# Kernel tuning notes

Hardware: AMD Instinct MI355X
Metric: run time of the kernel (lower is better)

## Reference

```python
import jax, jax.numpy as jnp
import numpy as np

B, S, NX, H = 8, 1024, 1024, 16
HD = NX // H  # head dim = 64
MASKED_BIAS = -10000.0


def setup_inputs() -> dict:
    key = jax.random.key(0)
    ks = jax.random.split(key, 6)
    return {
        "x": jax.random.normal(ks[0], (B, S, NX), dtype=jnp.float32),
        "query": jax.random.normal(ks[1], (B, S, NX), dtype=jnp.float32),
        "c_attn_w": jax.random.normal(ks[2], (NX, 3 * NX), dtype=jnp.float32) * 0.02,
        "c_attn_b": jnp.zeros((3 * NX,), dtype=jnp.float32),
        "c_proj_w": jax.random.normal(ks[3], (NX, NX), dtype=jnp.float32) * 0.02,
        "c_proj_b": jnp.zeros((NX,), dtype=jnp.float32),
    }


def _split_heads(t):
    # [B, S, NX] -> [B, H, S, HD]
    b, s, _ = t.shape
    return t.reshape(b, s, H, HD).transpose(0, 2, 1, 3)


def reference(x, query, c_attn_w, c_attn_b, c_proj_w, c_proj_b):
    # Conv1D: y = x @ W + b
    kv = x @ c_attn_w + c_attn_b          # [B,S,3NX]; use key/value slices
    qy = query @ c_attn_w + c_attn_b      # [B,S,3NX]; use query slice
    q = _split_heads(qy[..., :NX])                     # [B,H,S,HD]
    k = _split_heads(kv[..., NX:2 * NX])               # [B,H,S,HD]
    v = _split_heads(kv[..., 2 * NX:])                 # [B,H,S,HD]

    w = jnp.einsum("bhqd,bhkd->bhqk", q, k) / jnp.sqrt(jnp.float32(HD))
    causal = jnp.tril(jnp.ones((S, S), dtype=bool))[None, None]
    w = jnp.where(causal, w, jnp.float32(MASKED_BIAS))
    w = jax.nn.softmax(w, axis=-1)
    a = jnp.einsum("bhqk,bhkd->bhqd", w, v)            # [B,H,S,HD]
    a = a.transpose(0, 2, 1, 3).reshape(B, S, NX)      # merge heads
    return a @ c_proj_w + c_proj_b
```

## Files before the change

### kernel.cpp

```cpp
#include <hip/hip_runtime.h>
#include <cstdint>
#include <cstddef>

#define Bb   8
#define Ss   1024
#define NXx  1024
#define Hh   16
#define HDd  64
#define Mm   (Bb*Ss)

typedef __bf16 bf16x8 __attribute__((ext_vector_type(8)));
typedef float  f32x4  __attribute__((ext_vector_type(4)));

__device__ __forceinline__ unsigned short f2bf(float f) {
    union { float f; unsigned int u; } v; v.f = f;
    return (unsigned short)((v.u + 0x8000u) >> 16);
}

__device__ __forceinline__ unsigned cvt_pk_bf16(float lo, float hi) {
    unsigned r;
    asm("v_cvt_pk_bf16_f32 %0, %1, %2" : "=v"(r) : "v"(lo), "v"(hi));
    return r;
}

__device__ __forceinline__ void load_lds16(const unsigned short* g, unsigned short* lds_base) {
    __builtin_amdgcn_global_load_lds(
        (const __attribute__((address_space(1))) void*)g,
        (__attribute__((address_space(3))) void*)lds_base, 16, 0, 0);
}

__global__ __launch_bounds__(256) void prep(
    const float* __restrict__ x, const float* __restrict__ query,
    const float* __restrict__ caw, const float* __restrict__ cpw,
    unsigned short* __restrict__ xb, unsigned short* __restrict__ qb,
    unsigned short* __restrict__ Wt, unsigned short* __restrict__ Pt)
{
    __shared__ float tile[32][33];
    const int bid = blockIdx.x;
    const int tid = threadIdx.x;

    if (bid < 16384) {
        const float* in = (bid < 8192) ? x : query;
        unsigned short* out = (bid < 8192) ? xb : qb;
        const int i = ((bid & 8191) * 256 + tid) * 4;
        const float4 v = *(const float4*)(in + i);
        unsigned long long p = (unsigned long long)f2bf(v.x)
            | ((unsigned long long)f2bf(v.y) << 16)
            | ((unsigned long long)f2bf(v.z) << 32)
            | ((unsigned long long)f2bf(v.w) << 48);
        *(unsigned long long*)(out + i) = p;
        return;
    }

    const float* in;
    unsigned short* out;
    int C, t;
    if (bid < 16384 + 3072) { in = caw; out = Wt; C = 3072; t = bid - 16384; }
    else                    { in = cpw; out = Pt; C = 1024; t = bid - 19456; }
    const int ntx = C >> 5;
    const int c0 = (t % ntx) * 32, r0 = (t / ntx) * 32;
    const int tx = tid & 31, ty = tid >> 5;
    for (int i = ty; i < 32; i += 8)
        tile[i][tx] = in[(size_t)(r0 + i) * C + c0 + tx];
    __syncthreads();
    for (int i = ty; i < 32; i += 8)
        out[(size_t)(c0 + i) * 1024 + r0 + tx] = f2bf(tile[tx][i]);
}

__global__ __launch_bounds__(512, 4) void gemm256(
    const unsigned short* __restrict__ Ax,
    const unsigned short* __restrict__ Aq,
    const unsigned short* __restrict__ Bt,
    const float* __restrict__ bias,
    unsigned short* __restrict__ out_q,
    unsigned short* __restrict__ out_k,
    unsigned short* __restrict__ out_v)
{
    __shared__ unsigned short lds[36864];

    const int tid  = threadIdx.x;
    const int w    = tid >> 6;
    const int lane = tid & 63;
    const int wm   = (w >> 1) * 64;
    const int wn   = (w & 1) * 64;
    const int lrow = lane & 15;
    const int quad = lane >> 4;
    const int ph   = (quad ^ (lrow & 3) ^ (lrow >> 2)) & 3;

    const int n    = blockIdx.x;
    const int xcd  = n & 7;
    const int sg   = n >> 3;
    const int mi   = (xcd >> 1) * 8 + sg / 12;
    const int ni   = (xcd & 1) * 12 + sg % 12;
    const int m0   = mi << 8;
    const int n0   = ni << 7;
    const int region = n0 >> 10;
    const unsigned short* A = (region == 0) ? Aq : Ax;

    const int srow = lane >> 2;
    const int scol = (((lane & 3) ^ (srow & 3) ^ ((srow >> 2) & 3)) << 3);
    const unsigned short* pA0 = A  + (size_t)(m0 + w * 32 + srow) * 1024 + scol;
    const unsigned short* pA1 = A  + (size_t)(m0 + w * 32 + 16 + srow) * 1024 + scol;
    const unsigned short* pB0 = Bt + (size_t)(n0 + w * 16 + srow) * 1024 + scol;

    f32x4 acc[4][4] = {};

#pragma unroll
    for (int p = 0; p < 2; ++p) {
        const int bb = p * 12288;
        load_lds16(pA0, lds + bb + w * 1024);
        load_lds16(pA1, lds + bb + w * 1024 + 512);
        load_lds16(pB0, lds + bb + 8192 + w * 512);
        pA0 += 32; pA1 += 32; pB0 += 32;
    }
    asm volatile("s_waitcnt vmcnt(3)" ::: "memory");

    int cbuf = 0;
    int sbuf = 2;
#pragma unroll 1
    for (int t = 0; t < 32; ++t) {
        __builtin_amdgcn_s_barrier();
        asm volatile("" ::: "memory");
        if (t <= 29) {
            const int bb = sbuf * 12288;
            load_lds16(pA0, lds + bb + w * 1024);
            load_lds16(pA1, lds + bb + w * 1024 + 512);
            load_lds16(pB0, lds + bb + 8192 + w * 512);
            pA0 += 32; pA1 += 32; pB0 += 32;
        }

        const int rA = cbuf * 12288 + (wm + lrow) * 32 + ph * 8;
        const int rB = cbuf * 12288 + 8192 + (wn + lrow) * 32 + ph * 8;
        bf16x8 af[4], bq[4];
#pragma unroll
        for (int i = 0; i < 4; ++i) af[i] = *(const bf16x8*)&lds[rA + i * 512];
#pragma unroll
        for (int j = 0; j < 4; ++j) bq[j] = *(const bf16x8*)&lds[rB + j * 512];
        __builtin_amdgcn_s_setprio(1);
#pragma unroll
        for (int i = 0; i < 4; ++i)
#pragma unroll
            for (int j = 0; j < 4; ++j)
                acc[i][j] = __builtin_amdgcn_mfma_f32_16x16x32_bf16(af[i], bq[j], acc[i][j], 0, 0, 0);
        __builtin_amdgcn_s_setprio(0);

        if (t <= 29)      asm volatile("s_waitcnt vmcnt(3)" ::: "memory");
        else if (t == 30) asm volatile("s_waitcnt vmcnt(0)" ::: "memory");

        cbuf = (cbuf == 2) ? 0 : cbuf + 1;
        sbuf = (sbuf == 2) ? 0 : sbuf + 1;
    }

    __syncthreads();

    unsigned short* ep = lds + w * 2048;

    if (region != 2) {
        unsigned short* outp = (region == 0) ? out_q : out_k;
        const float sc = (region == 0) ? 0.125f : 1.0f;
#pragma unroll
        for (int j = 0; j < 4; ++j) {
            const float bv = bias[n0 + wn + j * 16 + lrow];
#pragma unroll
            for (int i = 0; i < 4; ++i)
#pragma unroll
                for (int r = 0; r < 4; ++r)
                    ep[(i * 16 + quad * 4 + r) * 24 + lrow] = f2bf((acc[i][j][r] + bv) * sc);
#pragma unroll
            for (int tt = 0; tt < 2; ++tt) {
                const int c    = tt * 64 + lane;
                const int row  = c >> 1, ch = (c & 1) * 8;
                const int mrow = m0 + wm + row;
                const int cc   = (n0 + wn + j * 16 + ch) & (NXx - 1);
                const int hh   = cc >> 6, dd = cc & 63;
                const int bh   = (mrow >> 10) * Hh + hh;
                const int ss   = mrow & (Ss - 1);
                *(uint4*)&outp[((size_t)bh * Ss + ss) * HDd + dd] =
                    *(const uint4*)&ep[row * 24 + ch];
            }
        }
    } else {
#pragma unroll
        for (int j = 0; j < 4; ++j) {
            const float bv = bias[n0 + wn + j * 16 + lrow];
#pragma unroll
            for (int i = 0; i < 4; ++i)
#pragma unroll
                for (int r = 0; r < 4; ++r)
                    ep[lrow * 72 + i * 16 + quad * 4 + r] = f2bf(acc[i][j][r] + bv);
#pragma unroll
            for (int tt = 0; tt < 2; ++tt) {
                const int c    = tt * 64 + lane;
                const int col  = c >> 3, rc = (c & 7) * 8;
                const int cc   = (n0 + wn + j * 16 + col) & (NXx - 1);
                const int hh   = cc >> 6, dd = cc & 63;
                const int mrow = m0 + wm + rc;
                const int bh   = (mrow >> 10) * Hh + hh;
                const int ss   = mrow & (Ss - 1);
                *(uint4*)&out_v[((size_t)bh * HDd + dd) * Ss + ss] =
                    *(const uint4*)&ep[col * 72 + rc];
            }
        }
    }
}

__global__ __launch_bounds__(512, 4) void gemmp(
    const unsigned short* __restrict__ A,
    const unsigned short* __restrict__ Bt,
    const float* __restrict__ bias,
    float* __restrict__ out_f)
{
    __shared__ unsigned short lds[24576];

    const int tid  = threadIdx.x;
    const int w    = tid >> 6;
    const int lane = tid & 63;
    const int wm   = (w >> 1) * 32;
    const int wn   = (w & 1) * 64;
    const int lrow = lane & 15;
    const int quad = lane >> 4;
    const int ph   = (quad ^ (lrow & 3) ^ (lrow >> 2)) & 3;

    const int n    = blockIdx.x;
    const int xcd  = n & 7;
    const int sg   = n >> 3;
    const int mi   = (xcd >> 1) * 16 + sg / 4;
    const int ni   = (xcd & 1) * 4 + (sg & 3);
    const int m0   = mi << 7;
    const int n0   = ni << 7;

    const int srow = lane >> 2;
    const int scol = (((lane & 3) ^ (srow & 3) ^ ((srow >> 2) & 3)) << 3);
    const unsigned short* pA0 = A  + (size_t)(m0 + w * 16 + srow) * 1024 + scol;
    const unsigned short* pB0 = Bt + (size_t)(n0 + w * 16 + srow) * 1024 + scol;

    f32x4 acc[2][4] = {};

#pragma unroll
    for (int p = 0; p < 2; ++p) {
        const int bb = p * 8192;
        load_lds16(pA0, lds + bb + w * 512);
        load_lds16(pB0, lds + bb + 4096 + w * 512);
        pA0 += 32; pB0 += 32;
    }
    asm volatile("s_waitcnt vmcnt(2)" ::: "memory");

    int cbuf = 0, sbuf = 2;
#pragma unroll 1
    for (int t = 0; t < 32; ++t) {
        __builtin_amdgcn_s_barrier();
        asm volatile("" ::: "memory");
        if (t <= 29) {
            const int bb = sbuf * 8192;
            load_lds16(pA0, lds + bb + w * 512);
            load_lds16(pB0, lds + bb + 4096 + w * 512);
            pA0 += 32; pB0 += 32;
        }

        const int rA = cbuf * 8192 + (wm + lrow) * 32 + ph * 8;
        const int rB = cbuf * 8192 + 4096 + (wn + lrow) * 32 + ph * 8;
        bf16x8 af[2], bq[4];
#pragma unroll
        for (int i = 0; i < 2; ++i) af[i] = *(const bf16x8*)&lds[rA + i * 512];
#pragma unroll
        for (int j = 0; j < 4; ++j) bq[j] = *(const bf16x8*)&lds[rB + j * 512];
        __builtin_amdgcn_s_setprio(1);
#pragma unroll
        for (int i = 0; i < 2; ++i)
#pragma unroll
            for (int j = 0; j < 4; ++j)
                acc[i][j] = __builtin_amdgcn_mfma_f32_16x16x32_bf16(af[i], bq[j], acc[i][j], 0, 0, 0);
        __builtin_amdgcn_s_setprio(0);

        if (t <= 29)      asm volatile("s_waitcnt vmcnt(2)" ::: "memory");
        else if (t == 30) asm volatile("s_waitcnt vmcnt(0)" ::: "memory");

        cbuf = (cbuf == 2) ? 0 : cbuf + 1;
        sbuf = (sbuf == 2) ? 0 : sbuf + 1;
    }

#pragma unroll
    for (int i = 0; i < 2; ++i)
#pragma unroll
        for (int j = 0; j < 4; ++j) {
            const int ncol = n0 + wn + j * 16 + lrow;
            const float bv = bias[ncol];
#pragma unroll
            for (int r = 0; r < 4; ++r) {
                const int mrow = m0 + wm + i * 16 + quad * 4 + r;
                out_f[(size_t)mrow * NXx + ncol] = acc[i][j][r] + bv;
            }
        }
}

__global__ __launch_bounds__(512) void flash_attn(
    const unsigned short* __restrict__ Qh,
    const unsigned short* __restrict__ Kh,
    const unsigned short* __restrict__ Vt,
    unsigned short* __restrict__ about)
{
    __shared__ unsigned short Ks[3][64][64];
    __shared__ unsigned short Vs[3][64][64];
    __shared__ unsigned short Pl[8][32][72];

    const int tid  = threadIdx.x;
    const int w    = tid >> 6;
    const int lane = tid & 63;
    const int bh   = blockIdx.x & 127;
    const int prg  = blockIdx.x >> 7;
    const int b    = bh >> 4, h = bh & 15;
    const int lrow = lane & 15;
    const int quad = lane >> 4;

    const unsigned short* Qb = Qh + (size_t)bh * Ss * HDd;
    const unsigned short* Kb = Kh + (size_t)bh * Ss * HDd;
    const unsigned short* Vb = Vt + (size_t)bh * HDd * Ss;

    const int sr = lane >> 3;
    const int lc = (((lane & 7) ^ sr) << 3);

    const int swz = lrow & 7;
    const int ca = ((quad ^ swz) << 3);
    const int cb = (((4 + quad) ^ swz) << 3);

    const int nkt0 = 4 * prg + 4;
    int qw = prg * 256 + w * 32;

    bf16x8 aq[2][2];
#pragma unroll
    for (int g = 0; g < 2; ++g)
#pragma unroll
        for (int c = 0; c < 2; ++c)
            aq[g][c] = *(const bf16x8*)(Qb + (size_t)(qw + g * 16 + lrow) * HDd + c * 32 + quad * 8);

    f32x4 O[2][4] = {};
    float lsum[2] = { 0.f, 0.f };

#pragma unroll
    for (int p = 0; p < 2; ++p) {
        load_lds16(Kb + (size_t)(p * 64 + w * 8 + sr) * HDd + lc, &Ks[p][w * 8][0]);
        load_lds16(Vb + (size_t)(w * 8 + sr) * Ss + p * 64 + lc,  &Vs[p][w * 8][0]);
    }
    asm volatile("s_waitcnt vmcnt(2)" ::: "memory");

    int cbuf = 0, sbuf = 2;
#pragma unroll 1
    for (int it = 0; it < 20; ++it) {
        __builtin_amdgcn_s_barrier();
        asm volatile("" ::: "memory");
        if (it <= 17) {
            const int itn = it + 2;
            const int k0n = (itn >= nkt0 ? itn - nkt0 : itn) * 64;
            load_lds16(Kb + (size_t)(k0n + w * 8 + sr) * HDd + lc, &Ks[sbuf][w * 8][0]);
            load_lds16(Vb + (size_t)(w * 8 + sr) * Ss + k0n + lc,  &Vs[sbuf][w * 8][0]);
        }

        if (it == nkt0) {
#pragma unroll
            for (int g = 0; g < 2; ++g) {
                float l = lsum[g];
                l += __shfl_xor(l, 16);
                l += __shfl_xor(l, 32);
                const float inv = 1.0f / l;
#pragma unroll
                for (int r = 0; r < 4; ++r) {
                    const float invr = __shfl(inv, quad * 4 + r);
                    const int q = qw + g * 16 + quad * 4 + r;
                    const size_t base = ((size_t)b * Ss + q) * NXx + h * HDd;
#pragma unroll
                    for (int f = 0; f < 4; ++f)
                        about[base + f * 16 + lrow] = f2bf(O[g][f][r] * invr);
                }
            }
            qw = (3 - prg) * 256 + w * 32;
#pragma unroll
            for (int g = 0; g < 2; ++g)
#pragma unroll
                for (int c = 0; c < 2; ++c)
                    aq[g][c] = *(const bf16x8*)(Qb + (size_t)(qw + g * 16 + lrow) * HDd + c * 32 + quad * 8);
#pragma unroll
            for (int g = 0; g < 2; ++g) {
                lsum[g] = 0.f;
#pragma unroll
                for (int f = 0; f < 4; ++f) O[g][f] = (f32x4){0.f, 0.f, 0.f, 0.f};
            }
        }

        const int k0 = (it >= nkt0 ? it - nkt0 : it) * 64;
        if (k0 <= qw + 31) {
            f32x4 st[2][4] = {};
#pragma unroll
            for (int j = 0; j < 4; ++j) {
                const bf16x8 kf0 = *(const bf16x8*)&Ks[cbuf][j * 16 + lrow][ca];
                const bf16x8 kf1 = *(const bf16x8*)&Ks[cbuf][j * 16 + lrow][cb];
                st[0][j] = __builtin_amdgcn_mfma_f32_16x16x32_bf16(kf0, aq[0][0], st[0][j], 0, 0, 0);
                st[0][j] = __builtin_amdgcn_mfma_f32_16x16x32_bf16(kf1, aq[0][1], st[0][j], 0, 0, 0);
                st[1][j] = __builtin_amdgcn_mfma_f32_16x16x32_bf16(kf0, aq[1][0], st[1][j], 0, 0, 0);
                st[1][j] = __builtin_amdgcn_mfma_f32_16x16x32_bf16(kf1, aq[1][1], st[1][j], 0, 0, 0);
            }

            const bool needMask = (k0 + 63 > qw);
#pragma unroll
            for (int g = 0; g < 2; ++g) {
                const int qg = qw + g * 16 + lrow;
#pragma unroll
                for (int j = 0; j < 4; ++j) {
                    const int kbase = k0 + j * 16 + quad * 4;
                    float e0 = __expf(st[g][j][0]);
                    float e1 = __expf(st[g][j][1]);
                    float e2 = __expf(st[g][j][2]);
                    float e3 = __expf(st[g][j][3]);
                    if (needMask) {
                        if (kbase     > qg) e0 = 0.f;
                        if (kbase + 1 > qg) e1 = 0.f;
                        if (kbase + 2 > qg) e2 = 0.f;
                        if (kbase + 3 > qg) e3 = 0.f;
                    }
                    lsum[g] += (e0 + e1) + (e2 + e3);
                    uint2 pk;
                    pk.x = cvt_pk_bf16(e0, e1);
                    pk.y = cvt_pk_bf16(e2, e3);
                    *(uint2*)&Pl[w][g * 16 + lrow][j * 16 + quad * 4] = pk;
                }
            }

            bf16x8 ap[2][2];
#pragma unroll
            for (int g = 0; g < 2; ++g)
#pragma unroll
                for (int c = 0; c < 2; ++c)
                    ap[g][c] = *(const bf16x8*)&Pl[w][g * 16 + lrow][c * 32 + quad * 8];
#pragma unroll
            for (int f = 0; f < 4; ++f) {
                const bf16x8 vf0 = *(const bf16x8*)&Vs[cbuf][f * 16 + lrow][ca];
                const bf16x8 vf1 = *(const bf16x8*)&Vs[cbuf][f * 16 + lrow][cb];
                O[0][f] = __builtin_amdgcn_mfma_f32_16x16x32_bf16(ap[0][0], vf0, O[0][f], 0, 0, 0);
                O[0][f] = __builtin_amdgcn_mfma_f32_16x16x32_bf16(ap[0][1], vf1, O[0][f], 0, 0, 0);
                O[1][f] = __builtin_amdgcn_mfma_f32_16x16x32_bf16(ap[1][0], vf0, O[1][f], 0, 0, 0);
                O[1][f] = __builtin_amdgcn_mfma_f32_16x16x32_bf16(ap[1][1], vf1, O[1][f], 0, 0, 0);
            }
        }

        if (it <= 17)      asm volatile("s_waitcnt vmcnt(2)" ::: "memory");
        else if (it == 18) asm volatile("s_waitcnt vmcnt(0)" ::: "memory");

        cbuf = (cbuf == 2) ? 0 : cbuf + 1;
        sbuf = (sbuf == 2) ? 0 : sbuf + 1;
    }

#pragma unroll
    for (int g = 0; g < 2; ++g) {
        float l = lsum[g];
        l += __shfl_xor(l, 16);
        l += __shfl_xor(l, 32);
        const float inv = 1.0f / l;
#pragma unroll
        for (int r = 0; r < 4; ++r) {
            const float invr = __shfl(inv, quad * 4 + r);
            const int q = qw + g * 16 + quad * 4 + r;
            const size_t base = ((size_t)b * Ss + q) * NXx + h * HDd;
#pragma unroll
            for (int f = 0; f < 4; ++f)
                about[base + f * 16 + lrow] = f2bf(O[g][f][r] * invr);
        }
    }
}

extern "C" void kernel_launch(void* const* d_in, const int* in_sizes, int n_in,
                              void* d_out, int out_size, void* d_ws, size_t ws_size,
                              hipStream_t stream) {
    const float* x        = (const float*)d_in[0];
    const float* query    = (const float*)d_in[1];
    const float* c_attn_w = (const float*)d_in[2];
    const float* c_attn_b = (const float*)d_in[3];
    const float* c_proj_w = (const float*)d_in[4];
    const float* c_proj_b = (const float*)d_in[5];
    float* out = (float*)d_out;

    const size_t nTok = (size_t)Mm * NXx;
    char* ws = (char*)d_ws;
    unsigned short* xb    = (unsigned short*)ws;                 ws += nTok * 2;
    unsigned short* qb    = (unsigned short*)ws;                 ws += nTok * 2;
    unsigned short* Wt    = (unsigned short*)ws;                 ws += (size_t)3 * NXx * NXx * 2;
    unsigned short* Pt    = (unsigned short*)ws;                 ws += (size_t)NXx * NXx * 2;
    unsigned short* Qh    = (unsigned short*)ws;                 ws += nTok * 2;
    unsigned short* Kh    = (unsigned short*)ws;                 ws += nTok * 2;
    unsigned short* Vt    = (unsigned short*)ws;                 ws += nTok * 2;
    unsigned short* about = (unsigned short*)ws;                 ws += nTok * 2;
    if ((size_t)(ws - (char*)d_ws) > ws_size) return;

    prep<<<20480, 256, 0, stream>>>(x, query, c_attn_w, c_proj_w, xb, qb, Wt, Pt);

    gemm256<<<768, 512, 0, stream>>>(xb, qb, Wt, c_attn_b, Qh, Kh, Vt);

    flash_attn<<<256, 512, 0, stream>>>(Qh, Kh, Vt, about);

    gemmp<<<512, 512, 0, stream>>>(about, Pt, c_proj_b, out);
}
```

Before: 262.2 us.

## Replace projection GEMM with 256-thread single-buffered kernel; move flash-attn waits before barrier

The output projection GEMM moves from a 512-thread, triple-buffered, 32-wide-K pipeline to a 256-thread kernel. Each wave now computes a 64x64 tile over K=64 steps, loading into a single XOR-swizzled LDS buffer between two __syncthreads. This gives more MFMA work per LDS load and fewer waves, but removes the overlap of global loads with compute. In flash attention, the vmcnt waits move before a second barrier placed after the prefetch issue, so the current tile is confirmed resident before compute. This adds a barrier per iteration.

```diff
diff --git a/kernel.cpp b/kernel.cpp
--- a/kernel.cpp
+++ b/kernel.cpp
@@ -204,83 +204,69 @@
     }
 }
 
-__global__ __launch_bounds__(512, 4) void gemmp(
+__global__ __launch_bounds__(256) void gemm128p(
     const unsigned short* __restrict__ A,
     const unsigned short* __restrict__ Bt,
     const float* __restrict__ bias,
     float* __restrict__ out_f)
 {
-    __shared__ unsigned short lds[24576];
+    __shared__ unsigned short smem[16384];
+    unsigned short (*As)[64] = (unsigned short (*)[64])(smem);
+    unsigned short (*Bs)[64] = (unsigned short (*)[64])(smem + 8192);
 
     const int tid  = threadIdx.x;
     const int w    = tid >> 6;
     const int lane = tid & 63;
-    const int wm   = (w >> 1) * 32;
+
+    const int n    = blockIdx.x;
+    const int xcd  = n & 7;
+    const int sgrp = n >> 3;
+    const int m0   = ((xcd >> 1) * 16 + sgrp / 4) * 128;
+    const int n0   = ((xcd & 1) * 4 + sgrp % 4) * 128;
+
+    const int wm   = (w >> 1) * 64;
     const int wn   = (w & 1) * 64;
     const int lrow = lane & 15;
     const int quad = lane >> 4;
-    const int ph   = (quad ^ (lrow & 3) ^ (lrow >> 2)) & 3;
-
-    const int n    = blockIdx.x;
-    const int xcd  = n & 7;
-    const int sg   = n >> 3;
-    const int mi   = (xcd >> 1) * 16 + sg / 4;
-    const int ni   = (xcd & 1) * 4 + (sg & 3);
-    const int m0   = mi << 7;
-    const int n0   = ni << 7;
-
-    const int srow = lane >> 2;
-    const int scol = (((lane & 3) ^ (srow & 3) ^ ((srow >> 2) & 3)) << 3);
-    const unsigned short* pA0 = A  + (size_t)(m0 + w * 16 + srow) * 1024 + scol;
-    const unsigned short* pB0 = Bt + (size_t)(n0 + w * 16 + srow) * 1024 + scol;
-
-    f32x4 acc[2][4] = {};
-
-#pragma unroll
-    for (int p = 0; p < 2; ++p) {
-        const int bb = p * 8192;
-        load_lds16(pA0, lds + bb + w * 512);
-        load_lds16(pB0, lds + bb + 4096 + w * 512);
-        pA0 += 32; pB0 += 32;
-    }
-    asm volatile("s_waitcnt vmcnt(2)" ::: "memory");
-
-    int cbuf = 0, sbuf = 2;
-#pragma unroll 1
-    for (int t = 0; t < 32; ++t) {
-        __builtin_amdgcn_s_barrier();
-        asm volatile("" ::: "memory");
-        if (t <= 29) {
-            const int bb = sbuf * 8192;
-            load_lds16(pA0, lds + bb + w * 512);
-            load_lds16(pB0, lds + bb + 4096 + w * 512);
-            pA0 += 32; pB0 += 32;
-        }
-
-        const int rA = cbuf * 8192 + (wm + lrow) * 32 + ph * 8;
-        const int rB = cbuf * 8192 + 4096 + (wn + lrow) * 32 + ph * 8;
-        bf16x8 af[2], bq[4];
-#pragma unroll
-        for (int i = 0; i < 2; ++i) af[i] = *(const bf16x8*)&lds[rA + i * 512];
-#pragma unroll
-        for (int j = 0; j < 4; ++j) bq[j] = *(const bf16x8*)&lds[rB + j * 512];
-        __builtin_amdgcn_s_setprio(1);
-#pragma unroll
-        for (int i = 0; i < 2; ++i)
-#pragma unroll
-            for (int j = 0; j < 4; ++j)
-                acc[i][j] = __builtin_amdgcn_mfma_f32_16x16x32_bf16(af[i], bq[j], acc[i][j], 0, 0, 0);
-        __builtin_amdgcn_s_setprio(0);
-
-        if (t <= 29)      asm volatile("s_waitcnt vmcnt(2)" ::: "memory");
-        else if (t == 30) asm volatile("s_waitcnt vmcnt(0)" ::: "memory");
-
-        cbuf = (cbuf == 2) ? 0 : cbuf + 1;
-        sbuf = (sbuf == 2) ? 0 : sbuf + 1;
-    }
-
-#pragma unroll
-    for (int i = 0; i < 2; ++i)
+
+    f32x4 acc[4][4] = {};
+
+    const int rr   = lane >> 3;
+    const int scol = (((lane & 7) ^ (lane >> 3)) << 3);
+    const unsigned short* Ag = A  + (size_t)(m0 + w * 32 + rr) * 1024 + scol;
+    const unsigned short* Bg = Bt + (size_t)(n0 + w * 32 + rr) * 1024 + scol;
+    unsigned short* ldsA = smem + (w * 32) * 64;
+    unsigned short* ldsB = smem + 8192 + (w * 32) * 64;
+
+    const int swz = lrow & 7;
+
+    for (int k0 = 0; k0 < 1024; k0 += 64) {
+        __syncthreads();
+#pragma unroll
+        for (int c = 0; c < 4; ++c) {
+            load_lds16(Ag + (size_t)(c * 8) * 1024 + k0, ldsA + c * 512);
+            load_lds16(Bg + (size_t)(c * 8) * 1024 + k0, ldsB + c * 512);
+        }
+        __syncthreads();
+#pragma unroll
+        for (int kk = 0; kk < 2; ++kk) {
+            bf16x8 af[4], bfr[4];
+            const int pc = (((kk * 4 + quad) ^ swz) << 3);
+#pragma unroll
+            for (int i = 0; i < 4; ++i) {
+                af[i]  = *(const bf16x8*)&As[wm + i * 16 + lrow][pc];
+                bfr[i] = *(const bf16x8*)&Bs[wn + i * 16 + lrow][pc];
+            }
+#pragma unroll
+            for (int i = 0; i < 4; ++i)
+#pragma unroll
+                for (int j = 0; j < 4; ++j)
+                    acc[i][j] = __builtin_amdgcn_mfma_f32_16x16x32_bf16(af[i], bfr[j], acc[i][j], 0, 0, 0);
+        }
+    }
+
+#pragma unroll
+    for (int i = 0; i < 4; ++i)
 #pragma unroll
         for (int j = 0; j < 4; ++j) {
             const int ncol = n0 + wn + j * 16 + lrow;
@@ -341,7 +327,6 @@
         load_lds16(Kb + (size_t)(p * 64 + w * 8 + sr) * HDd + lc, &Ks[p][w * 8][0]);
         load_lds16(Vb + (size_t)(w * 8 + sr) * Ss + p * 64 + lc,  &Vs[p][w * 8][0]);
     }
-    asm volatile("s_waitcnt vmcnt(2)" ::: "memory");
 
     int cbuf = 0, sbuf = 2;
 #pragma unroll 1
@@ -353,7 +338,14 @@
             const int k0n = (itn >= nkt0 ? itn - nkt0 : itn) * 64;
             load_lds16(Kb + (size_t)(k0n + w * 8 + sr) * HDd + lc, &Ks[sbuf][w * 8][0]);
             load_lds16(Vb + (size_t)(w * 8 + sr) * Ss + k0n + lc,  &Vs[sbuf][w * 8][0]);
-        }
+            asm volatile("s_waitcnt vmcnt(4)" ::: "memory");
+        } else if (it == 18) {
+            asm volatile("s_waitcnt vmcnt(2)" ::: "memory");
+        } else {
+            asm volatile("s_waitcnt vmcnt(0)" ::: "memory");
+        }
+        __builtin_amdgcn_s_barrier();
+        asm volatile("" ::: "memory");
 
         if (it == nkt0) {
 #pragma unroll
@@ -441,9 +433,6 @@
             }
         }
 
-        if (it <= 17)      asm volatile("s_waitcnt vmcnt(2)" ::: "memory");
-        else if (it == 18) asm volatile("s_waitcnt vmcnt(0)" ::: "memory");
-
         cbuf = (cbuf == 2) ? 0 : cbuf + 1;
         sbuf = (sbuf == 2) ? 0 : sbuf + 1;
     }
@@ -495,5 +484,5 @@
 
     flash_attn<<<256, 512, 0, stream>>>(Qh, Kh, Vt, about);
 
-    gemmp<<<512, 512, 0, stream>>>(about, Pt, c_proj_b, out);
-}
+    gemm128p<<<512, 256, 0, stream>>>(about, Pt, c_proj_b, out);
+}
```

Result: faster. 252.2 us (-3.8%).
